# Optimization experiments

Measured on AMD Instinct MI355X. Metric: run time of the kernel, lower is better.

## Reference

```python
import jax, jax.numpy as jnp
import numpy as np

B, FEAT, SFEAT, N, E = 64, 512, 128, 10000, 160000


def setup_inputs() -> dict:
    key = jax.random.key(0)
    ks = jax.random.split(key, 8)
    net = jax.random.normal(ks[0], (B, FEAT + SFEAT), dtype=jnp.float32)
    edge_index = jax.random.randint(ks[1], (2, E), 0, N, dtype=jnp.int64)
    s = 0.02
    return {
        "net": net,
        "edge_index": edge_index,
        "W_mlp2": jax.random.normal(ks[2], (FEAT + SFEAT, 2 * FEAT), dtype=jnp.float32) * s,
        "W_logr": jax.random.normal(ks[3], (FEAT, N * 3), dtype=jnp.float32) * s,
        "W_s": jax.random.normal(ks[4], (FEAT, N * 6), dtype=jnp.float32) * s,
        "W1_logr": jax.random.normal(ks[5], (3, 3), dtype=jnp.float32) * 0.3,
        "b1_logr": jnp.zeros((3,), jnp.float32),
        "W1_s": jax.random.normal(ks[6], (6, 6), dtype=jnp.float32) * 0.3,
        "b1_s": jnp.zeros((6,), jnp.float32),
        "W4_s": jax.random.normal(ks[7], (6, 6), dtype=jnp.float32) * 0.3,
        "b4_s": jnp.zeros((6,), jnp.float32),
    }


def gcn(x, src, dst, W, b):
    # GCNConv with added self-loops and symmetric normalization.
    # x: [B, N, C_in]; src/dst: [E+N] (self-loops pre-appended by caller)
    n = x.shape[1]
    deg = jax.ops.segment_sum(jnp.ones_like(dst, dtype=x.dtype), dst, num_segments=n)
    dinv = jnp.where(deg > 0, jax.lax.rsqrt(deg), 0.0)
    norm = dinv[src] * dinv[dst]  # [E+N]
    h = jnp.einsum("bnc,cd->bnd", x, W)  # transform first (C small)
    msg = h[:, src, :] * norm[None, :, None]  # gather + scale
    out = jnp.zeros_like(h).at[:, dst].add(msg)  # scatter-add over nodes
    return out + b


def reference(net, edge_index, W_mlp2, W_logr, W_s, W1_logr, b1_logr, W1_s, b1_s, W4_s, b4_s):
    loop = jnp.arange(N, dtype=edge_index.dtype)
    src = jnp.concatenate([edge_index[0], loop])
    dst = jnp.concatenate([edge_index[1], loop])

    net = jnp.tanh(net @ W_mlp2)  # [B, 2*FEAT]
    net_logr = jnp.tanh((net[:, :FEAT] @ W_logr).reshape(-1, N, 3))
    net_s = jnp.tanh((net[:, FEAT:2 * FEAT] @ W_s).reshape(-1, N, 6))

    net_logr = gcn(net_logr, src, dst, W1_logr, b1_logr)
    net_s = jnp.tanh(gcn(net_s, src, dst, W1_s, b1_s))
    net_s = gcn(net_s, src, dst, W4_s, b4_s)

    return jnp.concatenate([net_logr * 4.0, net_s * 50.0], axis=2)  # [B, N, 9]
```

## Files before the change

### kernel.cpp

```cpp
#include <hip/hip_runtime.h>
#include <math.h>

#define NNODE 10000
#define NEDGE 160000
#define BATCH 64
#define KDIM  512


__global__ void k_init_counts(int* counts) {
  int i = blockIdx.x * 256 + threadIdx.x;
  if (i < NNODE) counts[i] = 1;
}

__global__ void k_count(const int* __restrict__ ei, int* counts) {
  int e = blockIdx.x * 256 + threadIdx.x;
  if (e < NEDGE) atomicAdd(&counts[ei[NEDGE + e]], 1);
}

__global__ __launch_bounds__(1024) void k_scan(const int* __restrict__ counts,
                                               int* offs, int* cursor, float* dinv) {
  __shared__ int sd[1024];
  int t = threadIdx.x;
  int b0 = t * 10, b1 = b0 + 10;
  if (b1 > NNODE) b1 = NNODE;
  if (b0 > NNODE) b0 = NNODE;
  int s = 0;
  for (int i = b0; i < b1; i++) s += counts[i];
  sd[t] = s;
  __syncthreads();
  for (int off = 1; off < 1024; off <<= 1) {
    int v = (t >= off) ? sd[t - off] : 0;
    __syncthreads();
    sd[t] += v;
    __syncthreads();
  }
  int excl = (t == 0) ? 0 : sd[t - 1];
  for (int i = b0; i < b1; i++) {
    offs[i] = excl;
    cursor[i] = excl;
    dinv[i] = rsqrtf((float)counts[i]);
    excl += counts[i];
  }
  if (t == 1023) offs[NNODE] = sd[1023];
}

__global__ void k_fill(const int* __restrict__ ei, const float* __restrict__ dinv,
                       int* cursor, int* srcn, float* wnorm) {
  int e = blockIdx.x * 256 + threadIdx.x;
  if (e >= NEDGE + NNODE) return;
  int s, d;
  if (e < NEDGE) { s = ei[e]; d = ei[NEDGE + e]; }
  else           { s = e - NEDGE; d = s; }
  int pos = atomicAdd(&cursor[d], 1);
  srcn[pos] = s;
  wnorm[pos] = dinv[s] * dinv[d];
}


__global__ __launch_bounds__(256) void k_mlp2(const float* __restrict__ net,
                                              const float* __restrict__ W,
                                              float* __restrict__ net1) {
  __shared__ float a[640];
  int b = blockIdx.x, t = threadIdx.x;
  for (int i = t; i < 640; i += 256) a[i] = net[b * 640 + i];
  __syncthreads();
  float acc0 = 0.f, acc1 = 0.f, acc2 = 0.f, acc3 = 0.f;
  for (int k = 0; k < 640; k++) {
    float av = a[k];
    const float* Wr = W + k * 1024 + t;
    acc0 += av * Wr[0];
    acc1 += av * Wr[256];
    acc2 += av * Wr[512];
    acc3 += av * Wr[768];
  }
  float* o = net1 + b * 1024 + t;
  o[0]   = tanhf(acc0);
  o[256] = tanhf(acc1);
  o[512] = tanhf(acc2);
  o[768] = tanhf(acc3);
}


template <int C>
__global__ __launch_bounds__(192) void k_gemm(const float* __restrict__ A,
                                              const float* __restrict__ W,
                                              float* __restrict__ H, int NC) {
  constexpr int NODE_F = 64 * C;
  constexpr int NODE_P = NODE_F + 4;
  constexpr int NTILE  = 96 / C;
  constexpr int LDSA   = 64 * 68;
  constexpr int LDSF   = (NTILE * NODE_P > LDSA) ? NTILE * NODE_P : LDSA;
  __shared__ float lds[LDSF];
  float* As = lds;

  int tid = threadIdx.x;
  int tc = tid % 24, tr = tid / 24;
  int c0 = blockIdx.x * 96;
  int cw = c0 + tc * 4;
  int cwc = min(cw, NC - 4);

  float acc[8][4];
#pragma unroll
  for (int i = 0; i < 8; i++)
#pragma unroll
    for (int j = 0; j < 4; j++) acc[i][j] = 0.f;

  for (int kc = 0; kc < KDIM; kc += 64) {
    __syncthreads();
    for (int idx = tid; idx < 64 * 64; idx += 192) {
      int r = idx >> 6, kk = idx & 63;
      As[r * 68 + kk] = A[r * 1024 + kc + kk];
    }
    __syncthreads();
#pragma unroll 2
    for (int k = 0; k < 64; k += 4) {
      const float* Wp = W + (size_t)(kc + k) * NC + cwc;
      float4 w0 = *(const float4*)(Wp);
      float4 w1 = *(const float4*)(Wp + NC);
      float4 w2 = *(const float4*)(Wp + 2 * (size_t)NC);
      float4 w3 = *(const float4*)(Wp + 3 * (size_t)NC);
#pragma unroll
      for (int i = 0; i < 8; i++) {
        const float4 av = *(const float4*)&As[(tr + 8 * i) * 68 + k];
        acc[i][0] += av.x * w0.x + av.y * w1.x + av.z * w2.x + av.w * w3.x;
        acc[i][1] += av.x * w0.y + av.y * w1.y + av.z * w2.y + av.w * w3.y;
        acc[i][2] += av.x * w0.z + av.y * w1.z + av.z * w2.z + av.w * w3.z;
        acc[i][3] += av.x * w0.w + av.y * w1.w + av.z * w2.w + av.w * w3.w;
      }
    }
  }
  __syncthreads();

  int nact = min(96, NC - c0);
#pragma unroll
  for (int j = 0; j < 4; j++) {
    int cl = tc * 4 + j;
    if (cl < nact) {
      int nl = cl / C, ccl = cl % C;
      float* lp = lds + nl * NODE_P + ccl;
#pragma unroll
      for (int i = 0; i < 8; i++) {
        int b = tr + 8 * i;
        lp[b * C] = tanhf(acc[i][j]);
      }
    }
  }
  __syncthreads();

  int region = nact * 64;
  float* Hb = H + (size_t)c0 * 64;
  for (int f = tid * 4; f < region; f += 192 * 4) {
    int n = f / NODE_F, rem = f - n * NODE_F;
    const float4 v = *(const float4*)&lds[n * NODE_P + rem];
    *(float4*)&Hb[f] = v;
  }
}


template <int C>
__global__ void k_transform(const float* __restrict__ x, const float* __restrict__ Wc,
                            float* __restrict__ y) {
  int idx = blockIdx.x * 256 + threadIdx.x;
  if (idx >= NNODE * BATCH) return;
  float xi[C];
  const float* xp = x + (size_t)idx * C;
#pragma unroll
  for (int c = 0; c < C; c++) xi[c] = xp[c];
  float* yp = y + (size_t)idx * C;
#pragma unroll
  for (int d = 0; d < C; d++) {
    float s = 0.f;
#pragma unroll
    for (int c = 0; c < C; c++) s += xi[c] * Wc[c * C + d];
    yp[d] = s;
  }
}


__global__ void k_gather(const float* __restrict__ h, const int* __restrict__ offs,
                         const int* __restrict__ srcn, const float* __restrict__ wn,
                         const float* __restrict__ bias, float* __restrict__ out,
                         int C, int mode, float scale, int outc0) {
  int n = blockIdx.x, t = threadIdx.x;
  int BC = blockDim.x;
  int beg = offs[n], end = offs[n + 1];
  float acc = 0.f;
  int k = beg;
  for (; k + 2 <= end; k += 2) {
    int s0 = srcn[k], s1 = srcn[k + 1];
    float w0 = wn[k], w1 = wn[k + 1];
    acc += w0 * h[(size_t)s0 * BC + t];
    acc += w1 * h[(size_t)s1 * BC + t];
  }
  if (k < end) acc += wn[k] * h[(size_t)srcn[k] * BC + t];
  int b = t / C, c = t - b * C;
  acc += bias[c];
  if (mode == 0) {
    out[(size_t)n * BC + t] = tanhf(acc);
  } else {
    out[(size_t)b * (NNODE * 9) + n * 9 + outc0 + c] = acc * scale;
  }
}


extern "C" void kernel_launch(void* const* d_in, const int* in_sizes, int n_in,
                              void* d_out, int out_size, void* d_ws, size_t ws_size,
                              hipStream_t stream) {
  const float* net     = (const float*)d_in[0];
  const int*   ei      = (const int*)d_in[1];
  const float* W_mlp2  = (const float*)d_in[2];
  const float* W_logr  = (const float*)d_in[3];
  const float* W_s     = (const float*)d_in[4];
  const float* W1_logr = (const float*)d_in[5];
  const float* b1_logr = (const float*)d_in[6];
  const float* W1_s    = (const float*)d_in[7];
  const float* b1_s    = (const float*)d_in[8];
  const float* W4_s    = (const float*)d_in[9];
  const float* b4_s    = (const float*)d_in[10];
  float* out = (float*)d_out;

  char* w = (char*)d_ws;
  auto carve = [&](size_t nbytes) {
    char* p = w;
    w += (nbytes + 255) & ~(size_t)255;
    return p;
  };
  int*   counts = (int*)  carve(NNODE * 4);
  int*   offs   = (int*)  carve((NNODE + 1) * 4);
  int*   cursor = (int*)  carve(NNODE * 4);
  float* dinv   = (float*)carve(NNODE * 4);
  int*   srcn   = (int*)  carve((NEDGE + NNODE) * 4);
  float* wnorm  = (float*)carve((NEDGE + NNODE) * 4);
  float* net1   = (float*)carve(BATCH * 1024 * 4);
  float* Hlogr  = (float*)carve((size_t)NNODE * BATCH * 3 * 4);
  float* hA     = (float*)carve((size_t)NNODE * BATCH * 3 * 4);
  float* Hs     = (float*)carve((size_t)NNODE * BATCH * 6 * 4);
  float* hB     = (float*)carve((size_t)NNODE * BATCH * 6 * 4);
  float* tmid   = Hlogr;
  float* hC     = hB;

  k_init_counts<<<(NNODE + 255) / 256, 256, 0, stream>>>(counts);
  k_count<<<(NEDGE + 255) / 256, 256, 0, stream>>>(ei, counts);
  k_scan<<<1, 1024, 0, stream>>>(counts, offs, cursor, dinv);
  k_fill<<<(NEDGE + NNODE + 255) / 256, 256, 0, stream>>>(ei, dinv, cursor, srcn, wnorm);

  k_mlp2<<<BATCH, 256, 0, stream>>>(net, W_mlp2, net1);
  k_gemm<3><<<(30000 + 95) / 96, 192, 0, stream>>>(net1,       W_logr, Hlogr, 30000);
  k_gemm<6><<<(60000 + 95) / 96, 192, 0, stream>>>(net1 + 512, W_s,    Hs,    60000);

  k_transform<3><<<(NNODE * BATCH + 255) / 256, 256, 0, stream>>>(Hlogr, W1_logr, hA);
  k_gather<<<NNODE, 64 * 3, 0, stream>>>(hA, offs, srcn, wnorm, b1_logr, out, 3, 1, 4.0f, 0);

  k_transform<6><<<(NNODE * BATCH + 255) / 256, 256, 0, stream>>>(Hs, W1_s, hB);
  k_gather<<<NNODE, 64 * 6, 0, stream>>>(hB, offs, srcn, wnorm, b1_s, tmid, 6, 0, 1.0f, 0);

  k_transform<6><<<(NNODE * BATCH + 255) / 256, 256, 0, stream>>>(tmid, W4_s, hC);
  k_gather<<<NNODE, 64 * 6, 0, stream>>>(hC, offs, srcn, wnorm, b4_s, out, 6, 1, 50.0f, 3);
}
```

Measured before the change: 676.0 us.

## Fuse GCN transforms into GEMM epilogue and gathers, store features as bf16

Both large GEMMs are merged into one launch with smaller 48-column tiles. The per-node CxC GCN weight transform moves into the GEMM epilogue, and the second transform is folded into the middle gather together with the tanh. Intermediate node features are stored as bf16, which halves gather traffic at the cost of precision. The mlp2 kernel is also split across four times as many blocks. Together these drop three transform kernels and their full-size fp32 intermediate round trips.

New measurement: 713.2 us. +5.5%, slower.

```diff
diff --git a/kernel.cpp b/kernel.cpp
--- a/kernel.cpp
+++ b/kernel.cpp
@@ -5,6 +5,15 @@
 #define NEDGE 160000
 #define BATCH 64
 #define KDIM  512
+
+__device__ __forceinline__ unsigned short f2bf(float x) {
+  union { float f; unsigned u; } v; v.f = x;
+  return (unsigned short)((v.u + 0x7FFF + ((v.u >> 16) & 1)) >> 16);
+}
+__device__ __forceinline__ float bf2f(unsigned short h) {
+  union { unsigned u; float f; } v; v.u = ((unsigned)h) << 16;
+  return v.f;
+}
 
 
 __global__ void k_init_counts(int* counts) {
@@ -61,47 +70,34 @@
                                               const float* __restrict__ W,
                                               float* __restrict__ net1) {
   __shared__ float a[640];
-  int b = blockIdx.x, t = threadIdx.x;
-  for (int i = t; i < 640; i += 256) a[i] = net[b * 640 + i];
-  __syncthreads();
-  float acc0 = 0.f, acc1 = 0.f, acc2 = 0.f, acc3 = 0.f;
-  for (int k = 0; k < 640; k++) {
-    float av = a[k];
-    const float* Wr = W + k * 1024 + t;
-    acc0 += av * Wr[0];
-    acc1 += av * Wr[256];
-    acc2 += av * Wr[512];
-    acc3 += av * Wr[768];
-  }
-  float* o = net1 + b * 1024 + t;
-  o[0]   = tanhf(acc0);
-  o[256] = tanhf(acc1);
-  o[512] = tanhf(acc2);
-  o[768] = tanhf(acc3);
+  int bb = blockIdx.x >> 2, cg = (blockIdx.x & 3) << 8;
+  int t = threadIdx.x;
+  for (int i = t; i < 640; i += 256) a[i] = net[bb * 640 + i];
+  __syncthreads();
+  float acc = 0.f;
+#pragma unroll 4
+  for (int k = 0; k < 640; k++) acc += a[k] * W[k * 1024 + cg + t];
+  net1[bb * 1024 + cg + t] = tanhf(acc);
 }
 
 
 template <int C>
-__global__ __launch_bounds__(192) void k_gemm(const float* __restrict__ A,
-                                              const float* __restrict__ W,
-                                              float* __restrict__ H, int NC) {
+__device__ __forceinline__ void gemm_body(const float* __restrict__ A,
+                                          const float* __restrict__ W,
+                                          const float* __restrict__ W1,
+                                          float* lds, float* w1sh,
+                                          unsigned short* __restrict__ Hout,
+                                          int NC, int blk) {
   constexpr int NODE_F = 64 * C;
   constexpr int NODE_P = NODE_F + 4;
-  constexpr int NTILE  = 96 / C;
-  constexpr int LDSA   = 64 * 68;
-  constexpr int LDSF   = (NTILE * NODE_P > LDSA) ? NTILE * NODE_P : LDSA;
-  __shared__ float lds[LDSF];
-  float* As = lds;
-
   int tid = threadIdx.x;
-  int tc = tid % 24, tr = tid / 24;
-  int c0 = blockIdx.x * 96;
-  int cw = c0 + tc * 4;
-  int cwc = min(cw, NC - 4);
-
-  float acc[8][4];
-#pragma unroll
-  for (int i = 0; i < 8; i++)
+  if (tid < C * C) w1sh[tid] = W1[tid];
+  int tc = tid % 12, tr = tid / 12;
+  int c0 = blk * 48;
+
+  float acc[4][4];
+#pragma unroll
+  for (int i = 0; i < 4; i++)
 #pragma unroll
     for (int j = 0; j < 4; j++) acc[i][j] = 0.f;
 
@@ -109,19 +105,19 @@
     __syncthreads();
     for (int idx = tid; idx < 64 * 64; idx += 192) {
       int r = idx >> 6, kk = idx & 63;
-      As[r * 68 + kk] = A[r * 1024 + kc + kk];
+      lds[r * 68 + kk] = A[r * 1024 + kc + kk];
     }
     __syncthreads();
 #pragma unroll 2
     for (int k = 0; k < 64; k += 4) {
-      const float* Wp = W + (size_t)(kc + k) * NC + cwc;
+      const float* Wp = W + (size_t)(kc + k) * NC + c0 + tc * 4;
       float4 w0 = *(const float4*)(Wp);
       float4 w1 = *(const float4*)(Wp + NC);
       float4 w2 = *(const float4*)(Wp + 2 * (size_t)NC);
       float4 w3 = *(const float4*)(Wp + 3 * (size_t)NC);
 #pragma unroll
-      for (int i = 0; i < 8; i++) {
-        const float4 av = *(const float4*)&As[(tr + 8 * i) * 68 + k];
+      for (int i = 0; i < 4; i++) {
+        const float4 av = *(const float4*)&lds[(tr + 16 * i) * 68 + k];
         acc[i][0] += av.x * w0.x + av.y * w1.x + av.z * w2.x + av.w * w3.x;
         acc[i][1] += av.x * w0.y + av.y * w1.y + av.z * w2.y + av.w * w3.y;
         acc[i][2] += av.x * w0.z + av.y * w1.z + av.z * w2.z + av.w * w3.z;
@@ -131,75 +127,101 @@
   }
   __syncthreads();
 
-  int nact = min(96, NC - c0);
 #pragma unroll
   for (int j = 0; j < 4; j++) {
     int cl = tc * 4 + j;
-    if (cl < nact) {
-      int nl = cl / C, ccl = cl % C;
-      float* lp = lds + nl * NODE_P + ccl;
-#pragma unroll
-      for (int i = 0; i < 8; i++) {
-        int b = tr + 8 * i;
-        lp[b * C] = tanhf(acc[i][j]);
-      }
-    }
-  }
-  __syncthreads();
-
-  int region = nact * 64;
-  float* Hb = H + (size_t)c0 * 64;
-  for (int f = tid * 4; f < region; f += 192 * 4) {
-    int n = f / NODE_F, rem = f - n * NODE_F;
-    const float4 v = *(const float4*)&lds[n * NODE_P + rem];
-    *(float4*)&Hb[f] = v;
-  }
+    int nl = cl / C, ccl = cl % C;
+    float* lp = lds + nl * NODE_P + ccl;
+#pragma unroll
+    for (int i = 0; i < 4; i++) {
+      int b = tr + 16 * i;
+      lp[b * C] = tanhf(acc[i][j]);
+    }
+  }
+  __syncthreads();
+
+  unsigned short* Hb = Hout + (size_t)c0 * 64;
+  for (int f = tid * 4; f < 48 * 64; f += 192 * 4) {
+    float vals[4];
+#pragma unroll
+    for (int e = 0; e < 4; e++) {
+      int idx = f + e;
+      int n = idx / NODE_F, rem = idx - n * NODE_F;
+      int b = rem / C, d = rem - b * C;
+      const float* row = lds + n * NODE_P + b * C;
+      float v = 0.f;
+#pragma unroll
+      for (int c = 0; c < C; c++) v += row[c] * w1sh[c * C + d];
+      vals[e] = v;
+    }
+    ushort4 o;
+    o.x = f2bf(vals[0]); o.y = f2bf(vals[1]);
+    o.z = f2bf(vals[2]); o.w = f2bf(vals[3]);
+    *(ushort4*)&Hb[f] = o;
+  }
+}
+
+__global__ __launch_bounds__(192) void k_gemm_both(const float* __restrict__ net1,
+                                                   const float* __restrict__ W_logr,
+                                                   const float* __restrict__ W_s,
+                                                   const float* __restrict__ W1_logr,
+                                                   const float* __restrict__ W1_s,
+                                                   unsigned short* __restrict__ hA,
+                                                   unsigned short* __restrict__ hB) {
+  extern __shared__ float lds[];
+  __shared__ float w1sh[36];
+  int blk = blockIdx.x;
+  if (blk < 1250) gemm_body<6>(net1 + 512, W_s, W1_s, lds, w1sh, hB, 60000, blk);
+  else            gemm_body<3>(net1, W_logr, W1_logr, lds, w1sh, hA, 30000, blk - 1250);
 }
 
 
 template <int C>
-__global__ void k_transform(const float* __restrict__ x, const float* __restrict__ Wc,
-                            float* __restrict__ y) {
-  int idx = blockIdx.x * 256 + threadIdx.x;
-  if (idx >= NNODE * BATCH) return;
-  float xi[C];
-  const float* xp = x + (size_t)idx * C;
-#pragma unroll
-  for (int c = 0; c < C; c++) xi[c] = xp[c];
-  float* yp = y + (size_t)idx * C;
-#pragma unroll
-  for (int d = 0; d < C; d++) {
-    float s = 0.f;
-#pragma unroll
-    for (int c = 0; c < C; c++) s += xi[c] * Wc[c * C + d];
-    yp[d] = s;
-  }
-}
-
-
-__global__ void k_gather(const float* __restrict__ h, const int* __restrict__ offs,
-                         const int* __restrict__ srcn, const float* __restrict__ wn,
-                         const float* __restrict__ bias, float* __restrict__ out,
-                         int C, int mode, float scale, int outc0) {
+__global__ __launch_bounds__(64 * C) void k_gather_out(const unsigned short* __restrict__ h,
+    const int* __restrict__ offs, const int* __restrict__ srcn,
+    const float* __restrict__ wn, const float* __restrict__ bias,
+    float* __restrict__ out, float scale, int outc0) {
+  constexpr int BC = 64 * C;
   int n = blockIdx.x, t = threadIdx.x;
-  int BC = blockDim.x;
   int beg = offs[n], end = offs[n + 1];
   float acc = 0.f;
   int k = beg;
   for (; k + 2 <= end; k += 2) {
     int s0 = srcn[k], s1 = srcn[k + 1];
     float w0 = wn[k], w1 = wn[k + 1];
-    acc += w0 * h[(size_t)s0 * BC + t];
-    acc += w1 * h[(size_t)s1 * BC + t];
-  }
-  if (k < end) acc += wn[k] * h[(size_t)srcn[k] * BC + t];
+    acc += w0 * bf2f(h[(size_t)s0 * BC + t]);
+    acc += w1 * bf2f(h[(size_t)s1 * BC + t]);
+  }
+  if (k < end) acc += wn[k] * bf2f(h[(size_t)srcn[k] * BC + t]);
   int b = t / C, c = t - b * C;
-  acc += bias[c];
-  if (mode == 0) {
-    out[(size_t)n * BC + t] = tanhf(acc);
-  } else {
-    out[(size_t)b * (NNODE * 9) + n * 9 + outc0 + c] = acc * scale;
-  }
+  out[(size_t)b * (NNODE * 9) + n * 9 + outc0 + c] = (acc + bias[c]) * scale;
+}
+
+__global__ __launch_bounds__(384) void k_gather_mid(const unsigned short* __restrict__ h,
+    const int* __restrict__ offs, const int* __restrict__ srcn,
+    const float* __restrict__ wn, const float* __restrict__ b1,
+    const float* __restrict__ W4, unsigned short* __restrict__ hC) {
+  __shared__ float sd[384];
+  __shared__ float w4[36];
+  int n = blockIdx.x, t = threadIdx.x;
+  if (t < 36) w4[t] = W4[t];
+  int beg = offs[n], end = offs[n + 1];
+  float acc = 0.f;
+  int k = beg;
+  for (; k + 2 <= end; k += 2) {
+    int s0 = srcn[k], s1 = srcn[k + 1];
+    float w0 = wn[k], w1 = wn[k + 1];
+    acc += w0 * bf2f(h[(size_t)s0 * 384 + t]);
+    acc += w1 * bf2f(h[(size_t)s1 * 384 + t]);
+  }
+  if (k < end) acc += wn[k] * bf2f(h[(size_t)srcn[k] * 384 + t]);
+  int b = t / 6, c = t - b * 6;
+  sd[t] = tanhf(acc + b1[c]);
+  __syncthreads();
+  float o = 0.f;
+#pragma unroll
+  for (int c2 = 0; c2 < 6; c2++) o += sd[b * 6 + c2] * w4[c2 * 6 + c];
+  hC[(size_t)n * 384 + t] = f2bf(o);
 }
 
 
@@ -225,35 +247,27 @@
     w += (nbytes + 255) & ~(size_t)255;
     return p;
   };
-  int*   counts = (int*)  carve(NNODE * 4);
-  int*   offs   = (int*)  carve((NNODE + 1) * 4);
-  int*   cursor = (int*)  carve(NNODE * 4);
-  float* dinv   = (float*)carve(NNODE * 4);
-  int*   srcn   = (int*)  carve((NEDGE + NNODE) * 4);
-  float* wnorm  = (float*)carve((NEDGE + NNODE) * 4);
-  float* net1   = (float*)carve(BATCH * 1024 * 4);
-  float* Hlogr  = (float*)carve((size_t)NNODE * BATCH * 3 * 4);
-  float* hA     = (float*)carve((size_t)NNODE * BATCH * 3 * 4);
-  float* Hs     = (float*)carve((size_t)NNODE * BATCH * 6 * 4);
-  float* hB     = (float*)carve((size_t)NNODE * BATCH * 6 * 4);
-  float* tmid   = Hlogr;
-  float* hC     = hB;
+  int*            counts = (int*)           carve(NNODE * 4);
+  int*            offs   = (int*)           carve((NNODE + 1) * 4);
+  int*            cursor = (int*)           carve(NNODE * 4);
+  float*          dinv   = (float*)         carve(NNODE * 4);
+  int*            srcn   = (int*)           carve((NEDGE + NNODE) * 4);
+  float*          wnorm  = (float*)         carve((NEDGE + NNODE) * 4);
+  float*          net1   = (float*)         carve(BATCH * 1024 * 4);
+  unsigned short* hA     = (unsigned short*)carve((size_t)NNODE * BATCH * 3 * 2);
+  unsigned short* hB     = (unsigned short*)carve((size_t)NNODE * BATCH * 6 * 2);
+  unsigned short* hC     = (unsigned short*)carve((size_t)NNODE * BATCH * 6 * 2);
 
   k_init_counts<<<(NNODE + 255) / 256, 256, 0, stream>>>(counts);
   k_count<<<(NEDGE + 255) / 256, 256, 0, stream>>>(ei, counts);
   k_scan<<<1, 1024, 0, stream>>>(counts, offs, cursor, dinv);
   k_fill<<<(NEDGE + NNODE + 255) / 256, 256, 0, stream>>>(ei, dinv, cursor, srcn, wnorm);
 
-  k_mlp2<<<BATCH, 256, 0, stream>>>(net, W_mlp2, net1);
-  k_gemm<3><<<(30000 + 95) / 96, 192, 0, stream>>>(net1,       W_logr, Hlogr, 30000);
-  k_gemm<6><<<(60000 + 95) / 96, 192, 0, stream>>>(net1 + 512, W_s,    Hs,    60000);
-
-  k_transform<3><<<(NNODE * BATCH + 255) / 256, 256, 0, stream>>>(Hlogr, W1_logr, hA);
-  k_gather<<<NNODE, 64 * 3, 0, stream>>>(hA, offs, srcn, wnorm, b1_logr, out, 3, 1, 4.0f, 0);
-
-  k_transform<6><<<(NNODE * BATCH + 255) / 256, 256, 0, stream>>>(Hs, W1_s, hB);
-  k_gather<<<NNODE, 64 * 6, 0, stream>>>(hB, offs, srcn, wnorm, b1_s, tmid, 6, 0, 1.0f, 0);
-
-  k_transform<6><<<(NNODE * BATCH + 255) / 256, 256, 0, stream>>>(tmid, W4_s, hC);
-  k_gather<<<NNODE, 64 * 6, 0, stream>>>(hC, offs, srcn, wnorm, b4_s, out, 6, 1, 50.0f, 3);
-}
+  k_mlp2<<<256, 256, 0, stream>>>(net, W_mlp2, net1);
+  k_gemm_both<<<1875, 192, 17408, stream>>>(net1, W_logr, W_s, W1_logr, W1_s, hA, hB);
+
+  k_gather_out<3><<<NNODE, 192, 0, stream>>>(hA, offs, srcn, wnorm, b1_logr, out, 4.0f, 0);
+
+  k_gather_mid<<<NNODE, 384, 0, stream>>>(hB, offs, srcn, wnorm, b1_s, W4_s, hC);
+  k_gather_out<6><<<NNODE, 384, 0, stream>>>(hC, offs, srcn, wnorm, b4_s, out, 50.0f, 3);
+}
```
